# Kernel optimization log

Hardware: AMD Instinct MI355X
Metric: run time of the kernel (lower is better)

## Reference

```python
import jax, jax.numpy as jnp
import numpy as np

B, H, S, D = 2, 16, 2048, 64

def setup_inputs() -> dict:
    key = jax.random.key(0)
    kq, kk, kv = jax.random.split(key, 3)
    q = jax.random.normal(kq, (B, H, S, D), dtype=jnp.float32)
    k = jax.random.normal(kk, (B, H, S, D), dtype=jnp.float32)
    v = jax.random.normal(kv, (B, H, S, D), dtype=jnp.float32)
    mask = jnp.tril(jnp.ones((S, S), dtype=bool))  # causal, broadcast over B,H
    return {"q": q, "k": k, "v": v, "mask": mask}

def reference(q, k, v, mask):
    d_k = q.shape[-1]
    # [..., num_q, num_kv]
    qk = jnp.einsum('bhqd,bhkd->bhqk', q, k) / jnp.sqrt(jnp.asarray(d_k, q.dtype))
    qk = jnp.where(mask, qk, -jnp.inf)
    attn = jax.nn.softmax(qk, axis=-1)
    return jnp.einsum('bhqk,bhkd->bhqd', attn, v)
```

## Files before the change

### kernel.cpp

```cpp
#include <hip/hip_runtime.h>

#define SS 2048
#define DD 64
#define BH 32
#define QSCALE 0.1803368801f
#define BUFS 8448

typedef __attribute__((ext_vector_type(8))) short short8;
typedef __attribute__((ext_vector_type(4))) float floatx4;

__device__ __forceinline__ short f2bf(float x) {
  union { float f; unsigned u; } un; un.f = x;
  unsigned r = (un.u + 0x7FFFu + ((un.u >> 16) & 1u)) >> 16;
  return (short)r;
}
__device__ __forceinline__ short f2bf_fast(float x) {
  union { float f; unsigned u; } un; un.f = x;
  return (short)((un.u + 0x8000u) >> 16);
}
__device__ __forceinline__ float fexp2(float x) {
  return __builtin_amdgcn_exp2f(x);
}
__device__ __forceinline__ void gload16(const short* g, short* l) {
  __builtin_amdgcn_global_load_lds(
      (const __attribute__((address_space(1))) void*)g,
      (__attribute__((address_space(3))) void*)l, 16, 0, 0);
}
#define MFMA __builtin_amdgcn_mfma_f32_16x16x32_bf16

__device__ __forceinline__ int kperm(int c) {
  return (((c >> 2) & 1) << 4) + ((c >> 3) << 2) + (c & 3);
}

__global__ __launch_bounds__(256) void prep_kv(const float* __restrict__ K,
                                               const float* __restrict__ V,
                                               short* __restrict__ Kbf,
                                               short* __restrict__ Vtp) {
  __shared__ short Ts[64][72];
  const int bh = blockIdx.x;
  const int r0 = blockIdx.y * 64;
  const int t  = threadIdx.x;
  {
    const int r = t >> 2, c = (t & 3) * 16;
    const float* g = V + ((size_t)bh * SS + r0 + r) * DD + c;
    floatx4 a = *(const floatx4*)g;
    floatx4 b = *(const floatx4*)(g + 4);
    floatx4 cc = *(const floatx4*)(g + 8);
    floatx4 dd = *(const floatx4*)(g + 12);
    short8 x0, x1;
    x0[0]=f2bf(a[0]); x0[1]=f2bf(a[1]); x0[2]=f2bf(a[2]); x0[3]=f2bf(a[3]);
    x0[4]=f2bf(b[0]); x0[5]=f2bf(b[1]); x0[6]=f2bf(b[2]); x0[7]=f2bf(b[3]);
    x1[0]=f2bf(cc[0]);x1[1]=f2bf(cc[1]);x1[2]=f2bf(cc[2]);x1[3]=f2bf(cc[3]);
    x1[4]=f2bf(dd[0]);x1[5]=f2bf(dd[1]);x1[6]=f2bf(dd[2]);x1[7]=f2bf(dd[3]);
    *(short8*)&Ts[r][c] = x0;
    *(short8*)&Ts[r][c + 8] = x1;
  }
  {
    const size_t i = ((size_t)bh * SS + r0) * DD + (size_t)t * 16;
    floatx4 a = *(const floatx4*)(K + i);
    floatx4 b = *(const floatx4*)(K + i + 4);
    floatx4 cc = *(const floatx4*)(K + i + 8);
    floatx4 dd = *(const floatx4*)(K + i + 12);
    short8 x0, x1;
    x0[0]=f2bf(a[0]); x0[1]=f2bf(a[1]); x0[2]=f2bf(a[2]); x0[3]=f2bf(a[3]);
    x0[4]=f2bf(b[0]); x0[5]=f2bf(b[1]); x0[6]=f2bf(b[2]); x0[7]=f2bf(b[3]);
    x1[0]=f2bf(cc[0]);x1[1]=f2bf(cc[1]);x1[2]=f2bf(cc[2]);x1[3]=f2bf(cc[3]);
    x1[4]=f2bf(dd[0]);x1[5]=f2bf(dd[1]);x1[6]=f2bf(dd[2]);x1[7]=f2bf(dd[3]);
    *(short8*)(Kbf + i) = x0;
    *(short8*)(Kbf + i + 8) = x1;
  }
  __syncthreads();
  {
    const int d = t >> 2, cblk = (t & 3) * 16;
    short8 y0, y1;
    #pragma unroll
    for (int j = 0; j < 8; ++j) {
      const int c0 = cblk + j, c1 = cblk + 8 + j;
      y0[j] = Ts[(c0 & 32) + kperm(c0 & 31)][d];
      y1[j] = Ts[(c1 & 32) + kperm(c1 & 31)][d];
    }
    const int kt  = (r0 + cblk) >> 5;
    const int kin = cblk & 31;
    short* o = Vtp + (((size_t)bh * 64 + kt) * 64 + d) * 32 + kin;
    *(short8*)o = y0;
    *(short8*)(o + 8) = y1;
  }
}

__global__ __launch_bounds__(256, 4) void sdpa_fused(
    const float* __restrict__ Q, const short* __restrict__ Kbf,
    const short* __restrict__ Vtp, float* __restrict__ Og) {
  __shared__ __align__(16) short Sh[2][BUFS];

  const int tid  = threadIdx.x;
  const int w    = tid >> 6;
  const int lane = tid & 63;
  const int quad = lane >> 4;
  const int l16  = lane & 15;

  const int bh = blockIdx.x;
  const int y  = blockIdx.y;
  const int qt = (y < 8) ? (15 - y) : (y - 8);
  const int ktn = 4 * qt + 4;
  const int ktd = 4 * qt + w;
  const int qA  = qt * 128 + w * 32;
  const int qB  = qA + 16;

  const size_t base = (size_t)bh * SS * DD;
  const short* kbase = Kbf + base;
  const short* vtb   = Vtp + base;

  const int kso = (lane >> 3) * 64 + (((lane & 7) ^ (lane >> 3)) * 8);
  const int vso = (lane >> 2) * 32 + (((lane & 3) ^ ((lane >> 3) & 3)) * 8);

  {
    const short* gk = kbase + w * 512 + kso;
    gload16(gk,        &Sh[0][w * 544]);
    gload16(gk + 2048, &Sh[0][2176 + w * 544]);
    const short* gv = vtb + w * 512 + vso;
    gload16(gv,        &Sh[0][4352 + w * 512]);
    gload16(gv + 2048, &Sh[0][6400 + w * 512]);
  }

  short8 qaA0, qaA1, qaB0, qaB1;
  {
    const float* ga = Q + base + (size_t)(qA + l16) * DD + quad * 8;
    const float* gb = Q + base + (size_t)(qB + l16) * DD + quad * 8;
    floatx4 a0 = *(const floatx4*)ga,        a1 = *(const floatx4*)(ga + 4);
    floatx4 a2 = *(const floatx4*)(ga + 32), a3 = *(const floatx4*)(ga + 36);
    floatx4 b0 = *(const floatx4*)gb,        b1 = *(const floatx4*)(gb + 4);
    floatx4 b2 = *(const floatx4*)(gb + 32), b3 = *(const floatx4*)(gb + 36);
    #pragma unroll
    for (int j = 0; j < 4; ++j) {
      qaA0[j] = f2bf(a0[j] * QSCALE); qaA0[4 + j] = f2bf(a1[j] * QSCALE);
      qaA1[j] = f2bf(a2[j] * QSCALE); qaA1[4 + j] = f2bf(a3[j] * QSCALE);
      qaB0[j] = f2bf(b0[j] * QSCALE); qaB0[4 + j] = f2bf(b1[j] * QSCALE);
      qaB1[j] = f2bf(b2[j] * QSCALE); qaB1[4 + j] = f2bf(b3[j] * QSCALE);
    }
  }

  short8 ones;
  #pragma unroll
  for (int j = 0; j < 8; ++j) ones[j] = (short)0x3F80;

  floatx4 z = {0.f, 0.f, 0.f, 0.f};
  floatx4 oA0 = z, oA1 = z, oA2 = z, oA3 = z;
  floatx4 oB0 = z, oB1 = z, oB2 = z, oB3 = z;
  floatx4 sA = z, sB = z;

  const int kroA = (l16 >> 3) * 544 + (l16 & 7) * 64 + ((quad ^ (l16 & 7)) * 8);
  const int kroB = (l16 >> 3) * 544 + (l16 & 7) * 64 + (((quad + 4) ^ (l16 & 7)) * 8);
  const int vro  = l16 * 32 + ((quad ^ ((l16 >> 1) & 3)) * 8);

  int nb = 0;
  for (int ktp = 0; ktp < ktn; ktp += 2) {
    __asm__ volatile("s_waitcnt vmcnt(0)" ::: "memory");
    __syncthreads();

    if (ktp + 2 < ktn) {
      const short* gk = kbase + (size_t)(ktp + 2) * 2048 + w * 512 + kso;
      gload16(gk,        &Sh[nb ^ 1][w * 544]);
      gload16(gk + 2048, &Sh[nb ^ 1][2176 + w * 544]);
      const short* gv = vtb + (size_t)(ktp + 2) * 2048 + w * 512 + vso;
      gload16(gv,        &Sh[nb ^ 1][4352 + w * 512]);
      gload16(gv + 2048, &Sh[nb ^ 1][6400 + w * 512]);
    }

    #pragma unroll
    for (int j = 0; j < 2; ++j) {
      const int kt = ktp + j;
      if (kt <= ktd) {
        const short* lb = &Sh[nb][j * 2176];
        const short* vb = &Sh[nb][4352 + j * 2048];
        short8 kb00 = *(const short8*)(lb + kroA);
        short8 kb01 = *(const short8*)(lb + kroB);
        short8 kb10 = *(const short8*)(lb + kroA + 1088);
        short8 kb11 = *(const short8*)(lb + kroB + 1088);
        short8 vt0 = *(const short8*)(vb + vro);
        short8 vt1 = *(const short8*)(vb + vro + 512);
        short8 vt2 = *(const short8*)(vb + vro + 1024);
        short8 vt3 = *(const short8*)(vb + vro + 1536);

        floatx4 tA0 = z, tA1 = z, tB0 = z, tB1 = z;
        tA0 = MFMA(kb00, qaA0, tA0, 0, 0, 0); tA0 = MFMA(kb01, qaA1, tA0, 0, 0, 0);
        tA1 = MFMA(kb10, qaA0, tA1, 0, 0, 0); tA1 = MFMA(kb11, qaA1, tA1, 0, 0, 0);
        tB0 = MFMA(kb00, qaB0, tB0, 0, 0, 0); tB0 = MFMA(kb01, qaB1, tB0, 0, 0, 0);
        tB1 = MFMA(kb10, qaB0, tB1, 0, 0, 0); tB1 = MFMA(kb11, qaB1, tB1, 0, 0, 0);

        if (kt == ktd) {
          const int kq = quad * 4;
          #pragma unroll
          for (int r = 0; r < 4; ++r) {
            tA0[r] = (kq + r      <= l16)      ? tA0[r] : -1e30f;
            tA1[r] = (kq + r + 16 <= l16)      ? tA1[r] : -1e30f;
            tB0[r] = (kq + r      <= l16 + 16) ? tB0[r] : -1e30f;
            tB1[r] = (kq + r      <= l16)      ? tB1[r] : -1e30f;
          }
        }

        short8 paA, paB;
        #pragma unroll
        for (int r = 0; r < 4; ++r) {
          paA[r]     = f2bf_fast(fexp2(tA0[r]));
          paA[4 + r] = f2bf_fast(fexp2(tA1[r]));
          paB[r]     = f2bf_fast(fexp2(tB0[r]));
          paB[4 + r] = f2bf_fast(fexp2(tB1[r]));
        }

        sA = MFMA(ones, paA, sA, 0, 0, 0);
        sB = MFMA(ones, paB, sB, 0, 0, 0);

        oA0 = MFMA(vt0, paA, oA0, 0, 0, 0); oA1 = MFMA(vt1, paA, oA1, 0, 0, 0);
        oA2 = MFMA(vt2, paA, oA2, 0, 0, 0); oA3 = MFMA(vt3, paA, oA3, 0, 0, 0);
        oB0 = MFMA(vt0, paB, oB0, 0, 0, 0); oB1 = MFMA(vt1, paB, oB1, 0, 0, 0);
        oB2 = MFMA(vt2, paB, oB2, 0, 0, 0); oB3 = MFMA(vt3, paB, oB3, 0, 0, 0);
      }
    }
    nb ^= 1;
  }

  const float invA = 1.0f / sA[0];
  const float invB = 1.0f / sB[0];
  oA0 *= invA; oA1 *= invA; oA2 *= invA; oA3 *= invA;
  oB0 *= invB; oB1 *= invB; oB2 *= invB; oB3 *= invB;

  float* ra = Og + base + (size_t)(qA + l16) * DD + quad * 4;
  float* rb = Og + base + (size_t)(qB + l16) * DD + quad * 4;
  *(floatx4*)(ra)      = oA0;
  *(floatx4*)(ra + 16) = oA1;
  *(floatx4*)(ra + 32) = oA2;
  *(floatx4*)(ra + 48) = oA3;
  *(floatx4*)(rb)      = oB0;
  *(floatx4*)(rb + 16) = oB1;
  *(floatx4*)(rb + 32) = oB2;
  *(floatx4*)(rb + 48) = oB3;
}

extern "C" void kernel_launch(void* const* d_in, const int* in_sizes, int n_in,
                              void* d_out, int out_size, void* d_ws, size_t ws_size,
                              hipStream_t stream) {
  (void)in_sizes; (void)n_in; (void)out_size; (void)ws_size;
  const float* q = (const float*)d_in[0];
  const float* k = (const float*)d_in[1];
  const float* v = (const float*)d_in[2];
  float* o = (float*)d_out;

  short* Kbf = (short*)d_ws;
  short* Vtp = Kbf + (size_t)BH * SS * DD;

  prep_kv<<<dim3(BH, SS / 64), 256, 0, stream>>>(k, v, Kbf, Vtp);
  sdpa_fused<<<dim3(BH, 16), 256, 0, stream>>>(q, Kbf, Vtp, o);
}
```

Baseline: 134.8 us.

## Pair causal q-tiles per block with 8 waves and 4-tile K/V stages

```diff
diff --git a/kernel.cpp b/kernel.cpp
--- a/kernel.cpp
+++ b/kernel.cpp
@@ -4,7 +4,7 @@
 #define DD 64
 #define BH 32
 #define QSCALE 0.1803368801f
-#define BUFS 8448
+#define BUFS 16896
 
 typedef __attribute__((ext_vector_type(8))) short short8;
 typedef __attribute__((ext_vector_type(4))) float floatx4;
@@ -74,10 +74,10 @@
     const int d = t >> 2, cblk = (t & 3) * 16;
     short8 y0, y1;
     #pragma unroll
-    for (int j = 0; j < 8; ++j) {
-      const int c0 = cblk + j, c1 = cblk + 8 + j;
-      y0[j] = Ts[(c0 & 32) + kperm(c0 & 31)][d];
-      y1[j] = Ts[(c1 & 32) + kperm(c1 & 31)][d];
+    for (int jj = 0; jj < 8; ++jj) {
+      const int c0 = cblk + jj, c1 = cblk + 8 + jj;
+      y0[jj] = Ts[(c0 & 32) + kperm(c0 & 31)][d];
+      y1[jj] = Ts[(c1 & 32) + kperm(c1 & 31)][d];
     }
     const int kt  = (r0 + cblk) >> 5;
     const int kin = cblk & 31;
@@ -87,7 +87,45 @@
   }
 }
 
-__global__ __launch_bounds__(256, 4) void sdpa_fused(
+#define TILE_COMPUTE(JJ, MODE)                                               \
+  {                                                                          \
+    const short* lb = bufp + (JJ) * 2176;                                    \
+    const short* vb = bufp + 8704 + (JJ) * 2048;                             \
+    short8 kb00 = *(const short8*)(lb + kroA);                               \
+    short8 kb01 = *(const short8*)(lb + kroB);                               \
+    short8 kb10 = *(const short8*)(lb + kroA + 1088);                        \
+    short8 kb11 = *(const short8*)(lb + kroB + 1088);                        \
+    short8 vt0 = *(const short8*)(vb + vro);                                 \
+    short8 vt1 = *(const short8*)(vb + vro + 512);                           \
+    short8 vt2 = *(const short8*)(vb + vro + 1024);                          \
+    short8 vt3 = *(const short8*)(vb + vro + 1536);                          \
+    floatx4 t0 = z, t1 = z;                                                  \
+    t0 = MFMA(kb00, qa0, t0, 0, 0, 0); t0 = MFMA(kb01, qa1, t0, 0, 0, 0);    \
+    t1 = MFMA(kb10, qa0, t1, 0, 0, 0); t1 = MFMA(kb11, qa1, t1, 0, 0, 0);    \
+    if ((MODE) == 1) {                                                       \
+      _Pragma("unroll")                                                      \
+      for (int r = 0; r < 4; ++r) {                                          \
+        t0[r] = (quad * 4 + r <= l16) ? t0[r] : -1e30f;                      \
+        t1[r] = -1e30f;                                                      \
+      }                                                                      \
+    } else if ((MODE) == 2) {                                                \
+      _Pragma("unroll")                                                      \
+      for (int r = 0; r < 4; ++r) {                                          \
+        t1[r] = (quad * 4 + r <= l16) ? t1[r] : -1e30f;                      \
+      }                                                                      \
+    }                                                                        \
+    short8 pa;                                                               \
+    _Pragma("unroll")                                                        \
+    for (int r = 0; r < 4; ++r) {                                            \
+      pa[r]     = f2bf_fast(fexp2(t0[r]));                                   \
+      pa[4 + r] = f2bf_fast(fexp2(t1[r]));                                   \
+    }                                                                        \
+    sacc = MFMA(ones, pa, sacc, 0, 0, 0);                                    \
+    o0 = MFMA(vt0, pa, o0, 0, 0, 0); o1 = MFMA(vt1, pa, o1, 0, 0, 0);        \
+    o2 = MFMA(vt2, pa, o2, 0, 0, 0); o3 = MFMA(vt3, pa, o3, 0, 0, 0);        \
+  }
+
+__global__ __launch_bounds__(512, 2) void sdpa_fused(
     const float* __restrict__ Q, const short* __restrict__ Kbf,
     const short* __restrict__ Vtp, float* __restrict__ Og) {
   __shared__ __align__(16) short Sh[2][BUFS];
@@ -99,12 +137,7 @@
   const int l16  = lane & 15;
 
   const int bh = blockIdx.x;
-  const int y  = blockIdx.y;
-  const int qt = (y < 8) ? (15 - y) : (y - 8);
-  const int ktn = 4 * qt + 4;
-  const int ktd = 4 * qt + w;
-  const int qA  = qt * 128 + w * 32;
-  const int qB  = qA + 16;
+  const int jb = blockIdx.y;
 
   const size_t base = (size_t)bh * SS * DD;
   const short* kbase = Kbf + base;
@@ -112,128 +145,94 @@
 
   const int kso = (lane >> 3) * 64 + (((lane & 7) ^ (lane >> 3)) * 8);
   const int vso = (lane >> 2) * 32 + (((lane & 3) ^ ((lane >> 3) & 3)) * 8);
-
-  {
-    const short* gk = kbase + w * 512 + kso;
-    gload16(gk,        &Sh[0][w * 544]);
-    gload16(gk + 2048, &Sh[0][2176 + w * 544]);
-    const short* gv = vtb + w * 512 + vso;
-    gload16(gv,        &Sh[0][4352 + w * 512]);
-    gload16(gv + 2048, &Sh[0][6400 + w * 512]);
-  }
-
-  short8 qaA0, qaA1, qaB0, qaB1;
-  {
-    const float* ga = Q + base + (size_t)(qA + l16) * DD + quad * 8;
-    const float* gb = Q + base + (size_t)(qB + l16) * DD + quad * 8;
-    floatx4 a0 = *(const floatx4*)ga,        a1 = *(const floatx4*)(ga + 4);
-    floatx4 a2 = *(const floatx4*)(ga + 32), a3 = *(const floatx4*)(ga + 36);
-    floatx4 b0 = *(const floatx4*)gb,        b1 = *(const floatx4*)(gb + 4);
-    floatx4 b2 = *(const floatx4*)(gb + 32), b3 = *(const floatx4*)(gb + 36);
-    #pragma unroll
-    for (int j = 0; j < 4; ++j) {
-      qaA0[j] = f2bf(a0[j] * QSCALE); qaA0[4 + j] = f2bf(a1[j] * QSCALE);
-      qaA1[j] = f2bf(a2[j] * QSCALE); qaA1[4 + j] = f2bf(a3[j] * QSCALE);
-      qaB0[j] = f2bf(b0[j] * QSCALE); qaB0[4 + j] = f2bf(b1[j] * QSCALE);
-      qaB1[j] = f2bf(b2[j] * QSCALE); qaB1[4 + j] = f2bf(b3[j] * QSCALE);
-    }
-  }
-
-  short8 ones;
-  #pragma unroll
-  for (int j = 0; j < 8; ++j) ones[j] = (short)0x3F80;
-
-  floatx4 z = {0.f, 0.f, 0.f, 0.f};
-  floatx4 oA0 = z, oA1 = z, oA2 = z, oA3 = z;
-  floatx4 oB0 = z, oB1 = z, oB2 = z, oB3 = z;
-  floatx4 sA = z, sB = z;
-
   const int kroA = (l16 >> 3) * 544 + (l16 & 7) * 64 + ((quad ^ (l16 & 7)) * 8);
   const int kroB = (l16 >> 3) * 544 + (l16 & 7) * 64 + (((quad + 4) ^ (l16 & 7)) * 8);
   const int vro  = l16 * 32 + ((quad ^ ((l16 >> 1) & 3)) * 8);
 
-  int nb = 0;
-  for (int ktp = 0; ktp < ktn; ktp += 2) {
-    __asm__ volatile("s_waitcnt vmcnt(0)" ::: "memory");
-    __syncthreads();
-
-    if (ktp + 2 < ktn) {
-      const short* gk = kbase + (size_t)(ktp + 2) * 2048 + w * 512 + kso;
-      gload16(gk,        &Sh[nb ^ 1][w * 544]);
-      gload16(gk + 2048, &Sh[nb ^ 1][2176 + w * 544]);
-      const short* gv = vtb + (size_t)(ktp + 2) * 2048 + w * 512 + vso;
-      gload16(gv,        &Sh[nb ^ 1][4352 + w * 512]);
-      gload16(gv + 2048, &Sh[nb ^ 1][6400 + w * 512]);
-    }
-
-    #pragma unroll
-    for (int j = 0; j < 2; ++j) {
-      const int kt = ktp + j;
-      if (kt <= ktd) {
-        const short* lb = &Sh[nb][j * 2176];
-        const short* vb = &Sh[nb][4352 + j * 2048];
-        short8 kb00 = *(const short8*)(lb + kroA);
-        short8 kb01 = *(const short8*)(lb + kroB);
-        short8 kb10 = *(const short8*)(lb + kroA + 1088);
-        short8 kb11 = *(const short8*)(lb + kroB + 1088);
-        short8 vt0 = *(const short8*)(vb + vro);
-        short8 vt1 = *(const short8*)(vb + vro + 512);
-        short8 vt2 = *(const short8*)(vb + vro + 1024);
-        short8 vt3 = *(const short8*)(vb + vro + 1536);
-
-        floatx4 tA0 = z, tA1 = z, tB0 = z, tB1 = z;
-        tA0 = MFMA(kb00, qaA0, tA0, 0, 0, 0); tA0 = MFMA(kb01, qaA1, tA0, 0, 0, 0);
-        tA1 = MFMA(kb10, qaA0, tA1, 0, 0, 0); tA1 = MFMA(kb11, qaA1, tA1, 0, 0, 0);
-        tB0 = MFMA(kb00, qaB0, tB0, 0, 0, 0); tB0 = MFMA(kb01, qaB1, tB0, 0, 0, 0);
-        tB1 = MFMA(kb10, qaB0, tB1, 0, 0, 0); tB1 = MFMA(kb11, qaB1, tB1, 0, 0, 0);
-
-        if (kt == ktd) {
-          const int kq = quad * 4;
-          #pragma unroll
-          for (int r = 0; r < 4; ++r) {
-            tA0[r] = (kq + r      <= l16)      ? tA0[r] : -1e30f;
-            tA1[r] = (kq + r + 16 <= l16)      ? tA1[r] : -1e30f;
-            tB0[r] = (kq + r      <= l16 + 16) ? tB0[r] : -1e30f;
-            tB1[r] = (kq + r      <= l16)      ? tB1[r] : -1e30f;
+  const int wt = w >> 1, wc = w & 1;
+  const size_t gso = (size_t)wt * 2048 + wc * 1024;
+  const int dK = wt * 2176 + wc * 1088;
+  const int dV = 8704 + wt * 2048 + wc * 1024;
+
+  short8 ones;
+  #pragma unroll
+  for (int r = 0; r < 8; ++r) ones[r] = (short)0x3F80;
+  const floatx4 z = {0.f, 0.f, 0.f, 0.f};
+  const int hw = w >> 1;
+
+  for (int phase = 0; phase < 2; ++phase) {
+    const int qt = phase ? jb : (15 - jb);
+    const int np = qt + 1;
+    const int qA = qt * 128 + w * 16;
+
+    {
+      const short* gk = kbase + gso + kso;
+      gload16(gk,       &Sh[0][dK]);
+      gload16(gk + 512, &Sh[0][dK + 544]);
+      const short* gv = vtb + gso + vso;
+      gload16(gv,       &Sh[0][dV]);
+      gload16(gv + 512, &Sh[0][dV + 512]);
+    }
+
+    short8 qa0, qa1;
+    {
+      const float* ga = Q + base + (size_t)(qA + l16) * DD + quad * 8;
+      floatx4 a0 = *(const floatx4*)ga,        a1 = *(const floatx4*)(ga + 4);
+      floatx4 a2 = *(const floatx4*)(ga + 32), a3 = *(const floatx4*)(ga + 36);
+      #pragma unroll
+      for (int r = 0; r < 4; ++r) {
+        qa0[r] = f2bf(a0[r] * QSCALE); qa0[4 + r] = f2bf(a1[r] * QSCALE);
+        qa1[r] = f2bf(a2[r] * QSCALE); qa1[4 + r] = f2bf(a3[r] * QSCALE);
+      }
+    }
+
+    floatx4 o0 = z, o1 = z, o2 = z, o3 = z;
+    floatx4 sacc = z;
+
+    int nb = 0;
+    for (int p = 0; p < np; ++p) {
+      __asm__ volatile("s_waitcnt vmcnt(0)" ::: "memory");
+      __syncthreads();
+      const short* bufp = Sh[nb];
+
+      if (p + 1 < np) {
+        {
+          const size_t go = (size_t)(p + 1) * 8192 + gso;
+          const short* gk = kbase + go + kso;
+          gload16(gk,       &Sh[nb ^ 1][dK]);
+          gload16(gk + 512, &Sh[nb ^ 1][dK + 544]);
+          const short* gv = vtb + go + vso;
+          gload16(gv,       &Sh[nb ^ 1][dV]);
+          gload16(gv + 512, &Sh[nb ^ 1][dV + 512]);
+        }
+        TILE_COMPUTE(0, 0)
+        TILE_COMPUTE(1, 0)
+        TILE_COMPUTE(2, 0)
+        TILE_COMPUTE(3, 0)
+      } else {
+        #pragma unroll
+        for (int jj = 0; jj < 4; ++jj) {
+          if (jj < hw) {
+            TILE_COMPUTE(jj, 0)
+          } else if (jj == hw) {
+            if (w & 1) { TILE_COMPUTE(jj, 2) }
+            else       { TILE_COMPUTE(jj, 1) }
           }
         }
-
-        short8 paA, paB;
-        #pragma unroll
-        for (int r = 0; r < 4; ++r) {
-          paA[r]     = f2bf_fast(fexp2(tA0[r]));
-          paA[4 + r] = f2bf_fast(fexp2(tA1[r]));
-          paB[r]     = f2bf_fast(fexp2(tB0[r]));
-          paB[4 + r] = f2bf_fast(fexp2(tB1[r]));
-        }
-
-        sA = MFMA(ones, paA, sA, 0, 0, 0);
-        sB = MFMA(ones, paB, sB, 0, 0, 0);
-
-        oA0 = MFMA(vt0, paA, oA0, 0, 0, 0); oA1 = MFMA(vt1, paA, oA1, 0, 0, 0);
-        oA2 = MFMA(vt2, paA, oA2, 0, 0, 0); oA3 = MFMA(vt3, paA, oA3, 0, 0, 0);
-        oB0 = MFMA(vt0, paB, oB0, 0, 0, 0); oB1 = MFMA(vt1, paB, oB1, 0, 0, 0);
-        oB2 = MFMA(vt2, paB, oB2, 0, 0, 0); oB3 = MFMA(vt3, paB, oB3, 0, 0, 0);
       }
-    }
-    nb ^= 1;
-  }
-
-  const float invA = 1.0f / sA[0];
-  const float invB = 1.0f / sB[0];
-  oA0 *= invA; oA1 *= invA; oA2 *= invA; oA3 *= invA;
-  oB0 *= invB; oB1 *= invB; oB2 *= invB; oB3 *= invB;
-
-  float* ra = Og + base + (size_t)(qA + l16) * DD + quad * 4;
-  float* rb = Og + base + (size_t)(qB + l16) * DD + quad * 4;
-  *(floatx4*)(ra)      = oA0;
-  *(floatx4*)(ra + 16) = oA1;
-  *(floatx4*)(ra + 32) = oA2;
-  *(floatx4*)(ra + 48) = oA3;
-  *(floatx4*)(rb)      = oB0;
-  *(floatx4*)(rb + 16) = oB1;
-  *(floatx4*)(rb + 32) = oB2;
-  *(floatx4*)(rb + 48) = oB3;
+      nb ^= 1;
+    }
+
+    const float inv = 1.0f / sacc[0];
+    o0 *= inv; o1 *= inv; o2 *= inv; o3 *= inv;
+    float* ra = Og + base + (size_t)(qA + l16) * DD + quad * 4;
+    *(floatx4*)(ra)      = o0;
+    *(floatx4*)(ra + 16) = o1;
+    *(floatx4*)(ra + 32) = o2;
+    *(floatx4*)(ra + 48) = o3;
+
+    if (phase == 0) __syncthreads();
+  }
 }
 
 extern "C" void kernel_launch(void* const* d_in, const int* in_sizes, int n_in,
@@ -249,5 +248,5 @@
   short* Vtp = Kbf + (size_t)BH * SS * DD;
 
   prep_kv<<<dim3(BH, SS / 64), 256, 0, stream>>>(k, v, Kbf, Vtp);
-  sdpa_fused<<<dim3(BH, 16), 256, 0, stream>>>(q, Kbf, Vtp, o);
-}
+  sdpa_fused<<<dim3(BH, 8), 512, 0, stream>>>(q, Kbf, Vtp, o);
+}
```

Measured after the change: 131.2 us. 2.7% less time.
